# Performance work log

Measured on AMD Instinct MI355X. Metric: run time of the kernel, lower is better.

## Reference

```python
import jax, jax.numpy as jnp
import numpy as np

K_MAX = 16
SCALE = 1.0 / (32 * 32)


def setup_inputs() -> dict:
    key = jax.random.key(0)
    k1, k2, k3 = jax.random.split(key, 3)
    B, C_in, C_out, H, W = 16, 32, 32, 256, 256
    x = jax.random.normal(k1, (B, C_in, H, W), dtype=jnp.float32)
    weights_real = SCALE * jax.random.normal(k2, (C_in, C_out, K_MAX, K_MAX), dtype=jnp.float32)
    weights_imag = SCALE * jax.random.normal(k3, (C_in, C_out, K_MAX, K_MAX), dtype=jnp.float32)
    return {"x": x, "weights_real": weights_real, "weights_imag": weights_imag}


def reference(x, weights_real, weights_imag):
    B, C, H, W = x.shape
    C_out = weights_real.shape[1]
    k = min(K_MAX, H, W // 2 + 1)
    x_ft = jnp.fft.rfft2(x, norm='ortho')                 # (B, C, H, W//2+1) complex64
    w = (weights_real + 1j * weights_imag)[:, :, :k, :k]  # (C, C_out, k, k)
    # Faithful to original einsum 'bijk,ijkm->bkm' with broadcast over the
    # size-1 i/j slices: sums x_ft over its ROW axis; x_ft's COLUMN index
    # becomes the output-block row index.
    S = jnp.sum(x_ft[:, :, :k, :k], axis=2)               # (B, C, k)  indexed by freq column
    blk = jnp.einsum('bir,iorc->borc', S, w)              # (B, C_out, k, k)
    out_ft = jnp.zeros((B, C_out, H, W // 2 + 1), dtype=x_ft.dtype)
    out_ft = out_ft.at[:, :, :k, :k].set(blk)
    return jnp.fft.irfft2(out_ft, s=(H, W), norm='ortho')
```

## Files before the change

### kernel.cpp

```cpp
#include <hip/hip_runtime.h>
#include <math.h>


#define TWO_PI_OVER_256 0.02454369260617026

__global__ __launch_bounds__(256) void k1_spectral_sum(
    const float* __restrict__ x, float* __restrict__ s_re, float* __restrict__ s_im)
{
    __shared__ float twc[256], tws[256];
    __shared__ float gre[256], gim[256];
    __shared__ float Pre[4][256], Pim[4][256];
    __shared__ float red_re[16][16], red_im[16][16];

    const int t = threadIdx.x;
    const int bi = blockIdx.x;

    {
        double a = TWO_PI_OVER_256 * (double)t;
        twc[t] = (float)cos(a);
        tws[t] = (float)sin(a);
    }
    __syncthreads();
    {
        float gr = 0.f, gi = 0.f;
        #pragma unroll
        for (int u = 0; u < 16; ++u) {
            int idx = (u * t) & 255;
            gr += twc[idx];
            gi -= tws[idx];
        }
        gre[t] = gr; gim[t] = gi;
    }
    __syncthreads();

    const float* img = x + (size_t)bi * 65536;
    const int cg = t & 63, rg = t >> 6;
    float4 pr = {0.f,0.f,0.f,0.f}, pi = {0.f,0.f,0.f,0.f};
    for (int h = rg; h < 256; h += 4) {
        const float4 xv = *(const float4*)(img + (h << 8) + (cg << 2));
        const float gr = gre[h], gi = gim[h];
        pr.x += gr * xv.x; pr.y += gr * xv.y; pr.z += gr * xv.z; pr.w += gr * xv.w;
        pi.x += gi * xv.x; pi.y += gi * xv.y; pi.z += gi * xv.z; pi.w += gi * xv.w;
    }
    *(float4*)&Pre[rg][cg << 2] = pr;
    *(float4*)&Pim[rg][cg << 2] = pi;
    __syncthreads();

    {
        const int v = t >> 4, j = t & 15;
        float ar = 0.f, ai = 0.f;
        #pragma unroll
        for (int m = 0; m < 16; ++m) {
            const int w = j + (m << 4);
            const float prr = Pre[0][w] + Pre[1][w] + Pre[2][w] + Pre[3][w];
            const float pii = Pim[0][w] + Pim[1][w] + Pim[2][w] + Pim[3][w];
            const int idx = (v * w) & 255;
            const float c = twc[idx], s = tws[idx];
            ar += prr * c + pii * s;
            ai += pii * c - prr * s;
        }
        red_re[v][j] = ar; red_im[v][j] = ai;
    }
    __syncthreads();
    if (t < 16) {
        float ar = 0.f, ai = 0.f;
        #pragma unroll
        for (int j = 0; j < 16; ++j) { ar += red_re[t][j]; ai += red_im[t][j]; }
        s_re[bi * 16 + t] = ar * (1.0f / 256.0f);
        s_im[bi * 16 + t] = ai * (1.0f / 256.0f);
    }
}

__global__ __launch_bounds__(256) void k2_coef(
    const float* __restrict__ wr, const float* __restrict__ wi,
    const float* __restrict__ s_re, const float* __restrict__ s_im,
    float* __restrict__ coef)
{
    __shared__ float twc[256], tws[256];
    __shared__ float Sre[32][16], Sim[32][16];
    __shared__ float Br[256], Bi[256];

    const int t = threadIdx.x;
    const int bo = blockIdx.x;
    const int b = bo >> 5, o = bo & 31;

    {
        double a = TWO_PI_OVER_256 * (double)t;
        twc[t] = (float)cos(a);
        tws[t] = (float)sin(a);
    }
    {
        const float* srp = s_re + b * 512;
        const float* sip = s_im + b * 512;
        ((float*)Sre)[t]       = srp[t];
        ((float*)Sre)[t + 256] = srp[t + 256];
        ((float*)Sim)[t]       = sip[t];
        ((float*)Sim)[t + 256] = sip[t + 256];
    }
    __syncthreads();

    {
        const int u = t >> 4;
        float br = 0.f, bim = 0.f;
        const float* wrp = wr + o * 256 + t;
        const float* wip = wi + o * 256 + t;
        #pragma unroll 8
        for (int i = 0; i < 32; ++i) {
            const float a_re = Sre[i][u], a_im = Sim[i][u];
            const float w_re = wrp[i * 8192], w_im = wip[i * 8192];
            br  += a_re * w_re - a_im * w_im;
            bim += a_re * w_im + a_im * w_re;
        }
        Br[t] = br; Bi[t] = bim;
    }
    __syncthreads();

    {
        const int v = t & 15, yg = t >> 4;
        float br[16], bim[16];
        #pragma unroll
        for (int u = 0; u < 16; ++u) { br[u] = Br[u * 16 + v]; bim[u] = Bi[u * 16 + v]; }
        const float scale = (v == 0) ? (1.0f / 256.0f) : (1.0f / 128.0f);
        for (int m = 0; m < 16; ++m) {
            const int y = yg * 16 + m;
            const float c1 = twc[y], s1 = tws[y];
            float gr = br[0], gi = bim[0];
            float cc = 1.f, cs = 0.f;
            #pragma unroll
            for (int u = 1; u < 16; ++u) {
                const float nc = cc * c1 - cs * s1;
                const float ns = cc * s1 + cs * c1;
                cc = nc; cs = ns;
                gr += br[u] * cc - bim[u] * cs;
                gi += br[u] * cs + bim[u] * cc;
            }
            float* cp = coef + (((size_t)bo * 256 + y) << 5);
            cp[v]      = gr * scale;
            cp[16 + v] = (v == 0) ? 0.f : (-gi * scale);
        }
    }
}

__global__ __launch_bounds__(256) void k3_synth(
    const float* __restrict__ coef, float* __restrict__ out)
{
    __shared__ float twc[256], tws[256];
    const int t = threadIdx.x;
    const int blk = blockIdx.x;
    const int bo = blk >> 2;
    const int y0 = (blk & 3) << 6;

    {
        double a = TWO_PI_OVER_256 * (double)t;
        twc[t] = (float)cos(a);
        tws[t] = (float)sin(a);
    }
    __syncthreads();

    float c[16], s[16];
    #pragma unroll
    for (int v = 0; v < 16; ++v) {
        const int idx = (v * t) & 255;
        c[v] = twc[idx];
        s[v] = tws[idx];
    }
    s[0] = 0.f;

    const float* cp = coef + ((size_t)bo * 256 + y0) * 32;
    float* op = out + (size_t)bo * 65536 + (size_t)y0 * 256 + t;
    for (int yy = 0; yy < 64; ++yy) {
        const float* p = cp + yy * 32;
        float acc = 0.f;
        #pragma unroll
        for (int v = 0; v < 16; ++v) {
            acc += p[v] * c[v];
            acc += p[v + 16] * s[v];
        }
        op[yy * 256] = acc;
    }
}

extern "C" void kernel_launch(void* const* d_in, const int* in_sizes, int n_in,
                              void* d_out, int out_size, void* d_ws, size_t ws_size,
                              hipStream_t stream) {
    (void)in_sizes; (void)n_in; (void)out_size; (void)ws_size;
    const float* x  = (const float*)d_in[0];
    const float* wr = (const float*)d_in[1];
    const float* wi = (const float*)d_in[2];
    float* out  = (float*)d_out;
    float* s_re = (float*)d_ws;
    float* s_im = s_re + 8192;
    float* coef = s_im + 8192;

    k1_spectral_sum<<<512, 256, 0, stream>>>(x, s_re, s_im);
    k2_coef<<<512, 256, 0, stream>>>(wr, wi, s_re, s_im, coef);
    k3_synth<<<2048, 256, 0, stream>>>(coef, out);
}
```

Measured before the change: 284.5 us.

## Fuse coefficient and synthesis kernels; split spectral sum into row chunks

The coefficient-computation kernel and the synthesis kernel become one, so the per-row coefficients live in shared memory and are no longer written to and read back from global memory. The first kernel is split into four row chunks per image, giving 2048 blocks instead of 512, and writes partial sums that the fused kernel adds together. In exchange, the channel-mixing step with the weights is recomputed in each of the four row-chunk blocks per (batch, output channel).

```diff
diff --git a/kernel.cpp b/kernel.cpp
--- a/kernel.cpp
+++ b/kernel.cpp
@@ -4,16 +4,18 @@
 
 #define TWO_PI_OVER_256 0.02454369260617026
 
-__global__ __launch_bounds__(256) void k1_spectral_sum(
-    const float* __restrict__ x, float* __restrict__ s_re, float* __restrict__ s_im)
+__global__ __launch_bounds__(256) void k1_partial(
+    const float* __restrict__ x, float* __restrict__ s_part)
 {
     __shared__ float twc[256], tws[256];
-    __shared__ float gre[256], gim[256];
+    __shared__ float gre[64], gim[64];
     __shared__ float Pre[4][256], Pim[4][256];
     __shared__ float red_re[16][16], red_im[16][16];
 
     const int t = threadIdx.x;
-    const int bi = blockIdx.x;
+    const int blk = blockIdx.x;
+    const int bi = blk >> 2, chunk = blk & 3;
+    const int y0 = chunk << 6;
 
     {
         double a = TWO_PI_OVER_256 * (double)t;
@@ -21,11 +23,12 @@
         tws[t] = (float)sin(a);
     }
     __syncthreads();
-    {
+    if (t < 64) {
+        const int h = y0 + t;
         float gr = 0.f, gi = 0.f;
         #pragma unroll
         for (int u = 0; u < 16; ++u) {
-            int idx = (u * t) & 255;
+            const int idx = (u * h) & 255;
             gr += twc[idx];
             gi -= tws[idx];
         }
@@ -33,12 +36,14 @@
     }
     __syncthreads();
 
-    const float* img = x + (size_t)bi * 65536;
+    const float* img = x + (size_t)bi * 65536 + (size_t)y0 * 256;
     const int cg = t & 63, rg = t >> 6;
     float4 pr = {0.f,0.f,0.f,0.f}, pi = {0.f,0.f,0.f,0.f};
-    for (int h = rg; h < 256; h += 4) {
-        const float4 xv = *(const float4*)(img + (h << 8) + (cg << 2));
-        const float gr = gre[h], gi = gim[h];
+    #pragma unroll 4
+    for (int k = 0; k < 16; ++k) {
+        const int hl = rg + (k << 2);
+        const float4 xv = *(const float4*)(img + (hl << 8) + (cg << 2));
+        const float gr = gre[hl], gi = gim[hl];
         pr.x += gr * xv.x; pr.y += gr * xv.y; pr.z += gr * xv.z; pr.w += gr * xv.w;
         pi.x += gi * xv.x; pi.y += gi * xv.y; pi.z += gi * xv.z; pi.w += gi * xv.w;
     }
@@ -66,22 +71,25 @@
         float ar = 0.f, ai = 0.f;
         #pragma unroll
         for (int j = 0; j < 16; ++j) { ar += red_re[t][j]; ai += red_im[t][j]; }
-        s_re[bi * 16 + t] = ar * (1.0f / 256.0f);
-        s_im[bi * 16 + t] = ai * (1.0f / 256.0f);
+        float* sp = s_part + (size_t)bi * 128 + chunk * 32;
+        sp[t]      = ar * (1.0f / 256.0f);
+        sp[t + 16] = ai * (1.0f / 256.0f);
     }
 }
 
-__global__ __launch_bounds__(256) void k2_coef(
+__global__ __launch_bounds__(256) void k23_synth(
     const float* __restrict__ wr, const float* __restrict__ wi,
-    const float* __restrict__ s_re, const float* __restrict__ s_im,
-    float* __restrict__ coef)
+    const float* __restrict__ s_part, float* __restrict__ out)
 {
     __shared__ float twc[256], tws[256];
     __shared__ float Sre[32][16], Sim[32][16];
     __shared__ float Br[256], Bi[256];
+    __shared__ __align__(16) float coef[64][36];
 
     const int t = threadIdx.x;
-    const int bo = blockIdx.x;
+    const int blk = blockIdx.x;
+    const int bo = blk >> 2;
+    const int y0 = (blk & 3) << 6;
     const int b = bo >> 5, o = bo & 31;
 
     {
@@ -90,12 +98,14 @@
         tws[t] = (float)sin(a);
     }
     {
-        const float* srp = s_re + b * 512;
-        const float* sip = s_im + b * 512;
-        ((float*)Sre)[t]       = srp[t];
-        ((float*)Sre)[t + 256] = srp[t + 256];
-        ((float*)Sim)[t]       = sip[t];
-        ((float*)Sim)[t + 256] = sip[t + 256];
+        const float* sb = s_part + (size_t)b * 4096;
+        #pragma unroll
+        for (int e = t; e < 512; e += 256) {
+            const int i = e >> 4, u = e & 15;
+            const float* p = sb + i * 128 + u;
+            Sre[i][u] = p[0] + p[32] + p[64] + p[96];
+            Sim[i][u] = p[16] + p[48] + p[80] + p[112];
+        }
     }
     __syncthreads();
 
@@ -116,13 +126,15 @@
     __syncthreads();
 
     {
-        const int v = t & 15, yg = t >> 4;
+        const int v = t & 15, slot = t >> 4;
         float br[16], bim[16];
         #pragma unroll
         for (int u = 0; u < 16; ++u) { br[u] = Br[u * 16 + v]; bim[u] = Bi[u * 16 + v]; }
         const float scale = (v == 0) ? (1.0f / 256.0f) : (1.0f / 128.0f);
-        for (int m = 0; m < 16; ++m) {
-            const int y = yg * 16 + m;
+        #pragma unroll
+        for (int m = 0; m < 4; ++m) {
+            const int r = slot * 4 + m;
+            const int y = y0 + r;
             const float c1 = twc[y], s1 = tws[y];
             float gr = br[0], gi = bim[0];
             float cc = 1.f, cs = 0.f;
@@ -134,26 +146,9 @@
                 gr += br[u] * cc - bim[u] * cs;
                 gi += br[u] * cs + bim[u] * cc;
             }
-            float* cp = coef + (((size_t)bo * 256 + y) << 5);
-            cp[v]      = gr * scale;
-            cp[16 + v] = (v == 0) ? 0.f : (-gi * scale);
+            coef[r][v]      = gr * scale;
+            coef[r][16 + v] = (v == 0) ? 0.f : (-gi * scale);
         }
-    }
-}
-
-__global__ __launch_bounds__(256) void k3_synth(
-    const float* __restrict__ coef, float* __restrict__ out)
-{
-    __shared__ float twc[256], tws[256];
-    const int t = threadIdx.x;
-    const int blk = blockIdx.x;
-    const int bo = blk >> 2;
-    const int y0 = (blk & 3) << 6;
-
-    {
-        double a = TWO_PI_OVER_256 * (double)t;
-        twc[t] = (float)cos(a);
-        tws[t] = (float)sin(a);
     }
     __syncthreads();
 
@@ -166,17 +161,22 @@
     }
     s[0] = 0.f;
 
-    const float* cp = coef + ((size_t)bo * 256 + y0) * 32;
     float* op = out + (size_t)bo * 65536 + (size_t)y0 * 256 + t;
-    for (int yy = 0; yy < 64; ++yy) {
-        const float* p = cp + yy * 32;
+    #pragma unroll 2
+    for (int r = 0; r < 64; ++r) {
+        const float4* crow = (const float4*)&coef[r][0];
         float acc = 0.f;
         #pragma unroll
-        for (int v = 0; v < 16; ++v) {
-            acc += p[v] * c[v];
-            acc += p[v + 16] * s[v];
+        for (int q = 0; q < 4; ++q) {
+            const float4 pc = crow[q];
+            acc += pc.x * c[q*4+0] + pc.y * c[q*4+1] + pc.z * c[q*4+2] + pc.w * c[q*4+3];
         }
-        op[yy * 256] = acc;
+        #pragma unroll
+        for (int q = 0; q < 4; ++q) {
+            const float4 ps = crow[4+q];
+            acc += ps.x * s[q*4+0] + ps.y * s[q*4+1] + ps.z * s[q*4+2] + ps.w * s[q*4+3];
+        }
+        op[r * 256] = acc;
     }
 }
 
@@ -187,12 +187,9 @@
     const float* x  = (const float*)d_in[0];
     const float* wr = (const float*)d_in[1];
     const float* wi = (const float*)d_in[2];
-    float* out  = (float*)d_out;
-    float* s_re = (float*)d_ws;
-    float* s_im = s_re + 8192;
-    float* coef = s_im + 8192;
+    float* out    = (float*)d_out;
+    float* s_part = (float*)d_ws;
 
-    k1_spectral_sum<<<512, 256, 0, stream>>>(x, s_re, s_im);
-    k2_coef<<<512, 256, 0, stream>>>(wr, wi, s_re, s_im, coef);
-    k3_synth<<<2048, 256, 0, stream>>>(coef, out);
+    k1_partial<<<2048, 256, 0, stream>>>(x, s_part);
+    k23_synth<<<2048, 256, 0, stream>>>(wr, wi, s_part, out);
 }
```

Measured after the change: 279.2 us. No clear change (-1.9%).
